# Performance work log

Measured on AMD Instinct MI355X. Metric: run time of the kernel, lower is better.

Reference implementation:

```python
import jax, jax.numpy as jnp
import numpy as np

N_NODES = 100000
N_EDGES = 3200000
D_IN = 256
D_HID = 256
D_OUT = 64


def setup_inputs() -> dict:
    key = jax.random.key(0)
    k1, k2, k3, k4 = jax.random.split(key, 4)
    x = jax.random.normal(k1, (N_NODES, D_IN), dtype=jnp.float32)
    edge_index = jax.random.randint(k2, (2, N_EDGES), 0, N_NODES, dtype=jnp.int32)
    W1 = jax.random.normal(k3, (D_IN, D_HID), dtype=jnp.float32) / np.sqrt(D_IN)
    b1 = jnp.zeros((D_HID,), dtype=jnp.float32)
    W2 = jax.random.normal(k4, (D_HID, D_OUT), dtype=jnp.float32) / np.sqrt(D_HID)
    b2 = jnp.zeros((D_OUT,), dtype=jnp.float32)
    return {"x": x, "edge_index": edge_index, "W1": W1, "b1": b1, "W2": W2, "b2": b2}


def _gcn_conv(x, src, dst, norm, W, b, n_nodes):
    # dense linear transform, then normalized scatter-add aggregation
    h = x @ W  # [N, out]
    msg = norm[:, None] * h[src]  # gather + scale, [E+N, out]
    out = jax.ops.segment_sum(msg, dst, num_segments=n_nodes)
    return out + b


def reference(x, edge_index, W1, b1, W2, b2):
    n = x.shape[0]
    # add self-loops (PyG GCNConv default)
    loops = jnp.arange(n, dtype=edge_index.dtype)
    src = jnp.concatenate([edge_index[0], loops])
    dst = jnp.concatenate([edge_index[1], loops])
    # symmetric normalization deg^{-1/2}[src] * deg^{-1/2}[dst]
    deg = jax.ops.segment_sum(jnp.ones_like(src, dtype=x.dtype), dst, num_segments=n)
    dinv = jnp.where(deg > 0, jax.lax.rsqrt(jnp.maximum(deg, 1.0)), 0.0)
    norm = dinv[src] * dinv[dst]

    h = _gcn_conv(x, src, dst, norm, W1, b1, n)
    h = jax.nn.relu(h)
    # dropout is identity at inference
    h = _gcn_conv(h, src, dst, norm, W2, b2, n)
    return jax.nn.log_softmax(h, axis=1)
```

## Files before the change

kernel.cpp:

```cpp
#include <hip/hip_runtime.h>
#include <hip/hip_bf16.h>


typedef __bf16 bf16;
typedef bf16 bf16x4 __attribute__((ext_vector_type(4)));
typedef bf16 bf16x8 __attribute__((ext_vector_type(8)));
typedef float f32x4 __attribute__((ext_vector_type(4)));
typedef signed char s8;

#define NBLK 256

__global__ __launch_bounds__(256) void k_b1(const int* __restrict__ edge, int E, int chunk,
                                            int NB, int* __restrict__ gcnt) {
    __shared__ int cnt[512];
    int tid = threadIdx.x;
    for (int i = tid; i < NB; i += 256) cnt[i] = 0;
    __syncthreads();
    int s = blockIdx.x * chunk, e = min(s + chunk, E);
    for (int i = s + tid; i < e; i += 256) atomicAdd(&cnt[edge[E + i] >> 9], 1);
    __syncthreads();
    for (int i = tid; i < NB; i += 256) gcnt[blockIdx.x * NB + i] = cnt[i];
}

__global__ void k_b2(const int* __restrict__ gcnt, int NB, int E, int* __restrict__ bstart) {
    __shared__ int col[256];
    int k = threadIdx.x;
    int sum = 0;
    if (k < NB)
        for (int b = 0; b < NBLK; ++b) sum += gcnt[b * NB + k];
    col[k] = sum;
    __syncthreads();
    for (int o = 1; o < 256; o <<= 1) {
        int v = (k >= o) ? col[k - o] : 0;
        __syncthreads();
        col[k] += v;
        __syncthreads();
    }
    if (k < NB) bstart[k] = col[k] - sum;
    if (k == 0) bstart[NB] = E;
}

__global__ void k_b2b(int* __restrict__ gcnt, int NB, const int* __restrict__ bstart) {
    __shared__ int col[256];
    int b = threadIdx.x;
    int k = blockIdx.x;
    int v = gcnt[b * NB + k];
    col[b] = v;
    __syncthreads();
    for (int o = 1; o < 256; o <<= 1) {
        int t = (b >= o) ? col[b - o] : 0;
        __syncthreads();
        col[b] += t;
        __syncthreads();
    }
    gcnt[b * NB + k] = bstart[k] + col[b] - v;
}

__global__ __launch_bounds__(256) void k_b3(const int* __restrict__ edge, int E, int chunk,
                                            int NB, const int* __restrict__ base,
                                            int* __restrict__ ebuf) {
    __shared__ int cnt[512];
    __shared__ int bs[512];
    int tid = threadIdx.x;
    for (int i = tid; i < NB; i += 256) {
        cnt[i] = 0;
        bs[i] = base[blockIdx.x * NB + i];
    }
    __syncthreads();
    int s = blockIdx.x * chunk, e = min(s + chunk, E);
    for (int i = s + tid; i < e; i += 256) {
        int sv = edge[i], dv = edge[E + i];
        int k = dv >> 9;
        int r = atomicAdd(&cnt[k], 1);
        ebuf[bs[k] + r] = sv | ((dv & 511) << 17);
    }
}

__global__ __launch_bounds__(256) void k_b45(const int* __restrict__ ebuf,
                                             const int* __restrict__ bstart,
                                             const float* __restrict__ scale, int n, int E,
                                             int NB, int* __restrict__ off,
                                             float* __restrict__ dinv,
                                             float* __restrict__ ws) {
    __shared__ int cnt[512];
    __shared__ int red[256];
    int tid = threadIdx.x;
    int k = blockIdx.x;
    cnt[tid] = 0;
    cnt[tid + 256] = 0;
    __syncthreads();
    int s = bstart[k], e = bstart[k + 1];
    for (int i = s + tid; i < e; i += 256) atomicAdd(&cnt[(ebuf[i] >> 17) & 511], 1);
    __syncthreads();
    int c0 = cnt[tid * 2], c1 = cnt[tid * 2 + 1];
    int sum = c0 + c1;
    red[tid] = sum;
    __syncthreads();
    for (int o = 1; o < 256; o <<= 1) {
        int v = (tid >= o) ? red[tid - o] : 0;
        __syncthreads();
        red[tid] += v;
        __syncthreads();
    }
    int ex = red[tid] - sum;
    int base = k << 9;
    int g0 = base + tid * 2, g1 = g0 + 1;
    int o0 = s + ex, o1 = s + ex + c0;
    if (g0 < n) {
        off[g0] = o0;
        float d0 = rsqrtf((float)(c0 + 1));
        dinv[g0] = d0;
        ws[g0] = d0 * scale[g0];
    } else if (g0 == n) off[g0] = o0;
    if (g1 < n) {
        off[g1] = o1;
        float d1 = rsqrtf((float)(c1 + 1));
        dinv[g1] = d1;
        ws[g1] = d1 * scale[g1];
    } else if (g1 == n) off[g1] = o1;
    if (k == NB - 1 && tid == 0) off[n] = E;
}

__global__ __launch_bounds__(256) void k_b6(const int* __restrict__ ebuf,
                                            const int* __restrict__ bstart,
                                            const int* __restrict__ off,
                                            const float* __restrict__ ws, int n,
                                            int2* __restrict__ pair) {
    __shared__ int cnt[512];
    __shared__ int offl[512];
    int tid = threadIdx.x;
    int k = blockIdx.x;
    int base = k << 9;
    cnt[tid] = 0;
    cnt[tid + 256] = 0;
    offl[tid] = (base + tid < n) ? off[base + tid] : 0;
    offl[tid + 256] = (base + 256 + tid < n) ? off[base + 256 + tid] : 0;
    __syncthreads();
    int s = bstart[k], e = bstart[k + 1];
    for (int i = s + tid; i < e; i += 256) {
        int pk = ebuf[i];
        int sv = pk & 0x1ffff;
        int node = (pk >> 17) & 511;
        int r = atomicAdd(&cnt[node], 1);
        pair[offl[node] + r] = make_int2(sv, __float_as_int(ws[sv]));
    }
}

__global__ __launch_bounds__(256) void k_quant(const float* __restrict__ x,
                                               unsigned char* __restrict__ xq,
                                               float* __restrict__ scale, int n) {
    int row = blockIdx.x * 4 + (threadIdx.x >> 6);
    int lane = threadIdx.x & 63;
    if (row >= n) return;
    f32x4 v = ((const f32x4*)x)[(size_t)row * 64 + lane];
    float m = fmaxf(fmaxf(fabsf(v[0]), fabsf(v[1])), fmaxf(fabsf(v[2]), fabsf(v[3])));
    for (int o = 32; o > 0; o >>= 1) m = fmaxf(m, __shfl_xor(m, o));
    m = fmaxf(m, 1e-20f);
    float inv = 127.0f / m;
    int b0 = (__float2int_rn(v[0] * inv) + 128) & 255;
    int b1 = (__float2int_rn(v[1] * inv) + 128) & 255;
    int b2 = (__float2int_rn(v[2] * inv) + 128) & 255;
    int b3 = (__float2int_rn(v[3] * inv) + 128) & 255;
    ((int*)xq)[(size_t)row * 64 + lane] = b0 | (b1 << 8) | (b2 << 16) | (b3 << 24);
    if (lane == 0) scale[row] = m / 127.0f;
}

__global__ __launch_bounds__(256) void k_quant2(const bf16* __restrict__ tb,
                                                const float* __restrict__ scale,
                                                unsigned char* __restrict__ tq,
                                                float* __restrict__ tscale,
                                                float* __restrict__ r2, int n) {
    int t = blockIdx.x * 256 + threadIdx.x;
    int row = t >> 3;
    int l8 = t & 7;
    if (row >= n) return;
    bf16x8 v = ((const bf16x8*)tb)[(size_t)row * 8 + l8];
    float f[8], m = 0.0f;
#pragma unroll
    for (int j = 0; j < 8; ++j) { f[j] = (float)v[j]; m = fmaxf(m, fabsf(f[j])); }
    for (int o = 4; o > 0; o >>= 1) m = fmaxf(m, __shfl_xor(m, o));
    m = fmaxf(m, 1e-20f);
    float inv = 127.0f / m;
    int lo = 0, hi = 0;
#pragma unroll
    for (int j = 0; j < 4; ++j) lo |= ((__float2int_rn(f[j] * inv) + 128) & 255) << (8 * j);
#pragma unroll
    for (int j = 0; j < 4; ++j) hi |= ((__float2int_rn(f[4 + j] * inv) + 128) & 255) << (8 * j);
    ((int2*)tq)[(size_t)row * 8 + l8] = make_int2(lo, hi);
    if (l8 == 0) {
        float s = m / 127.0f;
        tscale[row] = s;
        r2[row] = s / scale[row];
    }
}

__global__ void k_wt(const float* __restrict__ W, bf16* __restrict__ Wt, int NC) {
    int nc = blockIdx.x;
    int k = threadIdx.x;
    Wt[nc * 256 + k] = (bf16)W[k * NC + nc];
}

__device__ __forceinline__ void acc16(float a[16], uint4 t, float w, float& wsum) {
    wsum += w;
    unsigned u0 = t.x, u1 = t.y, u2 = t.z, u3 = t.w;
    a[0]  += w * (float)(u0 & 255u);
    a[1]  += w * (float)((u0 >> 8) & 255u);
    a[2]  += w * (float)((u0 >> 16) & 255u);
    a[3]  += w * (float)(u0 >> 24);
    a[4]  += w * (float)(u1 & 255u);
    a[5]  += w * (float)((u1 >> 8) & 255u);
    a[6]  += w * (float)((u1 >> 16) & 255u);
    a[7]  += w * (float)(u1 >> 24);
    a[8]  += w * (float)(u2 & 255u);
    a[9]  += w * (float)((u2 >> 8) & 255u);
    a[10] += w * (float)((u2 >> 16) & 255u);
    a[11] += w * (float)(u2 >> 24);
    a[12] += w * (float)(u3 & 255u);
    a[13] += w * (float)((u3 >> 8) & 255u);
    a[14] += w * (float)((u3 >> 16) & 255u);
    a[15] += w * (float)(u3 >> 24);
}

__device__ __forceinline__ void acc8(float a[8], int2 t, float w, float& wsum) {
    wsum += w;
    unsigned u0 = (unsigned)t.x, u1 = (unsigned)t.y;
    a[0] += w * (float)(u0 & 255u);
    a[1] += w * (float)((u0 >> 8) & 255u);
    a[2] += w * (float)((u0 >> 16) & 255u);
    a[3] += w * (float)(u0 >> 24);
    a[4] += w * (float)(u1 & 255u);
    a[5] += w * (float)((u1 >> 8) & 255u);
    a[6] += w * (float)((u1 >> 16) & 255u);
    a[7] += w * (float)(u1 >> 24);
}

__global__ __launch_bounds__(256) void k_agg1(const unsigned char* __restrict__ xq,
                                              const float* __restrict__ scale,
                                              const int* __restrict__ off,
                                              const int2* __restrict__ pair,
                                              const float* __restrict__ dinv,
                                              bf16* __restrict__ ax, int n) {
    int wv = blockIdx.x * 4 + (threadIdx.x >> 6);
    int lane = threadIdx.x & 63;
    int node = wv * 4 + (lane >> 4);
    int l16 = lane & 15;
    if (node >= n) return;
    int s0 = off[node], s1 = off[node + 1];
    float dv = dinv[node];
    float a[16] = {};
    float wsum = 0.0f;
    uint4 xs = *(const uint4*)(xq + (size_t)node * 256 + l16 * 16);
    acc16(a, xs, dv * scale[node], wsum);
    int e = s0;
    if (s1 - s0 >= 4) {
        int2 p[4];
#pragma unroll
        for (int q = 0; q < 4; ++q) p[q] = pair[s0 + q];
        e = s0 + 4;
        for (; e + 4 <= s1; e += 4) {
            uint4 t[4];
#pragma unroll
            for (int q = 0; q < 4; ++q)
                t[q] = *(const uint4*)(xq + (size_t)p[q].x * 256 + l16 * 16);
            int2 pn[4];
#pragma unroll
            for (int q = 0; q < 4; ++q) pn[q] = pair[e + q];
#pragma unroll
            for (int q = 0; q < 4; ++q) acc16(a, t[q], __int_as_float(p[q].y), wsum);
#pragma unroll
            for (int q = 0; q < 4; ++q) p[q] = pn[q];
        }
        uint4 t[4];
#pragma unroll
        for (int q = 0; q < 4; ++q)
            t[q] = *(const uint4*)(xq + (size_t)p[q].x * 256 + l16 * 16);
#pragma unroll
        for (int q = 0; q < 4; ++q) acc16(a, t[q], __int_as_float(p[q].y), wsum);
    }
    for (; e < s1; ++e) {
        int2 p = pair[e];
        uint4 t = *(const uint4*)(xq + (size_t)p.x * 256 + l16 * 16);
        acc16(a, t, __int_as_float(p.y), wsum);
    }
    float c = 128.0f * wsum;
    bf16x8 o0, o1;
#pragma unroll
    for (int j = 0; j < 8; ++j) o0[j] = (bf16)((a[j] - c) * dv);
#pragma unroll
    for (int j = 0; j < 8; ++j) o1[j] = (bf16)((a[8 + j] - c) * dv);
    ((bf16x8*)ax)[(size_t)node * 32 + l16 * 2] = o0;
    ((bf16x8*)ax)[(size_t)node * 32 + l16 * 2 + 1] = o1;
}

__device__ __forceinline__ int swz(int s) { return s ^ ((s >> 3) & 7); }

__global__ __launch_bounds__(256) void k_gemmp(const bf16* __restrict__ A,
                                               const bf16* __restrict__ Bt,
                                               const float* __restrict__ bias,
                                               bf16* __restrict__ C, int n) {
    __shared__ __align__(16) bf16 As[4 * 64 * 8];
    __shared__ __align__(16) bf16 Bs[16 * 64 * 8];
    int tid = threadIdx.x;
    int bm = blockIdx.x * 64;
    int w = tid >> 6, lane = tid & 63;

    int r = tid >> 2;
    int cq = tid & 3;
    int a_slot = swz(((r >> 4) * 64) + cq * 16 + (r & 15));
    int arow = bm + r; if (arow > n - 1) arow = n - 1;

    f32x4 acc[16] = {};

    for (int k0 = 0; k0 < 256; k0 += 32) {
        __syncthreads();
        uint4 av = *(const uint4*)(A + (size_t)arow * 256 + k0 + cq * 8);
        *(uint4*)(As + a_slot * 8) = av;
#pragma unroll
        for (int rep = 0; rep < 4; ++rep) {
            int r2 = rep * 64 + r;
            uint4 bv = *(const uint4*)(Bt + (size_t)r2 * 256 + k0 + cq * 8);
            *(uint4*)(Bs + swz(((r2 >> 4) * 64) + cq * 16 + (r2 & 15)) * 8) = bv;
        }
        __syncthreads();
        bf16x8 af = *(const bf16x8*)(As + swz(w * 64 + lane) * 8);
#pragma unroll
        for (int ct = 0; ct < 16; ++ct) {
            bf16x8 bfr = *(const bf16x8*)(Bs + swz(ct * 64 + lane) * 8);
            acc[ct] = __builtin_amdgcn_mfma_f32_16x16x32_bf16(af, bfr, acc[ct], 0, 0, 0);
        }
    }

    int colb = lane & 15, rowq = lane >> 4;
#pragma unroll
    for (int ct = 0; ct < 16; ++ct) {
        int col = ct * 16 + colb;
        float bv = bias[col];
#pragma unroll
        for (int rr = 0; rr < 4; ++rr) {
            int row = bm + w * 16 + rowq * 4 + rr;
            if (row < n) {
                float v = acc[ct][rr] + bv;
                C[(size_t)row * 256 + col] = (bf16)(v > 0.0f ? v : 0.0f);
            }
        }
    }
}

__global__ __launch_bounds__(256) void k_gemm2(const bf16* __restrict__ A,
                                               const bf16* __restrict__ Bt,
                                               bf16* __restrict__ C, int n) {
    __shared__ __align__(16) bf16 As[4 * 64 * 8];
    __shared__ __align__(16) bf16 Bs[4 * 64 * 8];
    int tid = threadIdx.x;
    int bm = blockIdx.x * 64;
    int w = tid >> 6, lane = tid & 63;
    int wm = w >> 1, wn = w & 1;

    int r = tid >> 2;
    int cq = tid & 3;
    int lds_slot = swz(((r >> 4) * 64) + cq * 16 + (r & 15));
    int arow = bm + r; if (arow > n - 1) arow = n - 1;

    f32x4 acc[2][2] = {};

    for (int k0 = 0; k0 < 256; k0 += 32) {
        __syncthreads();
        uint4 av = *(const uint4*)(A + (size_t)arow * 256 + k0 + cq * 8);
        uint4 bv = *(const uint4*)(Bt + (size_t)r * 256 + k0 + cq * 8);
        *(uint4*)(As + lds_slot * 8) = av;
        *(uint4*)(Bs + lds_slot * 8) = bv;
        __syncthreads();
#pragma unroll
        for (int i = 0; i < 2; ++i) {
            bf16x8 af = *(const bf16x8*)(As + swz((wm * 2 + i) * 64 + lane) * 8);
#pragma unroll
            for (int j = 0; j < 2; ++j) {
                bf16x8 bfr = *(const bf16x8*)(Bs + swz((wn * 2 + j) * 64 + lane) * 8);
                acc[i][j] = __builtin_amdgcn_mfma_f32_16x16x32_bf16(af, bfr, acc[i][j], 0, 0, 0);
            }
        }
    }

    int colb = lane & 15, rowq = lane >> 4;
#pragma unroll
    for (int i = 0; i < 2; ++i) {
#pragma unroll
        for (int j = 0; j < 2; ++j) {
            int col = wn * 32 + j * 16 + colb;
#pragma unroll
            for (int rr = 0; rr < 4; ++rr) {
                int row = bm + wm * 32 + i * 16 + rowq * 4 + rr;
                if (row < n) C[(size_t)row * 64 + col] = (bf16)acc[i][j][rr];
            }
        }
    }
}

__global__ __launch_bounds__(256) void k_agg2(const unsigned char* __restrict__ tq,
                                              const float* __restrict__ tscale,
                                              const float* __restrict__ r2,
                                              const int* __restrict__ off,
                                              const int2* __restrict__ pair,
                                              const float* __restrict__ dinv,
                                              const float* __restrict__ b2,
                                              float* __restrict__ out, int n) {
    int wv = blockIdx.x * 4 + (threadIdx.x >> 6);
    int lane = threadIdx.x & 63;
    int node = wv * 8 + (lane >> 3);
    int l8 = lane & 7;
    if (node >= n) return;
    int s0 = off[node], s1 = off[node + 1];
    float dv = dinv[node];
    const int2* T = (const int2*)tq;
    int2 ts = T[(size_t)node * 8 + l8];
    float a[8] = {};
    float wsum = 0.0f;
    acc8(a, ts, dv * tscale[node], wsum);
    int e = s0;
    if (s1 - s0 >= 4) {
        int2 p[4]; float sc[4];
#pragma unroll
        for (int q = 0; q < 4; ++q) p[q] = pair[s0 + q];
#pragma unroll
        for (int q = 0; q < 4; ++q) sc[q] = r2[p[q].x];
        e = s0 + 4;
        for (; e + 4 <= s1; e += 4) {
            int2 t[4];
#pragma unroll
            for (int q = 0; q < 4; ++q) t[q] = T[(size_t)p[q].x * 8 + l8];
            int2 pn[4];
#pragma unroll
            for (int q = 0; q < 4; ++q) pn[q] = pair[e + q];
            float scn[4];
#pragma unroll
            for (int q = 0; q < 4; ++q) scn[q] = r2[pn[q].x];
#pragma unroll
            for (int q = 0; q < 4; ++q) acc8(a, t[q], __int_as_float(p[q].y) * sc[q], wsum);
#pragma unroll
            for (int q = 0; q < 4; ++q) { p[q] = pn[q]; sc[q] = scn[q]; }
        }
        int2 t[4];
#pragma unroll
        for (int q = 0; q < 4; ++q) t[q] = T[(size_t)p[q].x * 8 + l8];
#pragma unroll
        for (int q = 0; q < 4; ++q) acc8(a, t[q], __int_as_float(p[q].y) * sc[q], wsum);
    }
    for (; e < s1; ++e) {
        int2 p = pair[e];
        float w = __int_as_float(p.y) * r2[p.x];
        int2 t = T[(size_t)p.x * 8 + l8];
        acc8(a, t, w, wsum);
    }
    float c = 128.0f * wsum;
    const float4* B2 = (const float4*)b2;
    float4 bv0 = B2[l8 * 2], bv1 = B2[l8 * 2 + 1];
    a[0] = (a[0] - c) * dv + bv0.x; a[1] = (a[1] - c) * dv + bv0.y;
    a[2] = (a[2] - c) * dv + bv0.z; a[3] = (a[3] - c) * dv + bv0.w;
    a[4] = (a[4] - c) * dv + bv1.x; a[5] = (a[5] - c) * dv + bv1.y;
    a[6] = (a[6] - c) * dv + bv1.z; a[7] = (a[7] - c) * dv + bv1.w;
    float m = a[0];
#pragma unroll
    for (int j = 1; j < 8; ++j) m = fmaxf(m, a[j]);
    for (int o = 4; o > 0; o >>= 1) m = fmaxf(m, __shfl_xor(m, o));
    float s = 0.0f;
#pragma unroll
    for (int j = 0; j < 8; ++j) s += __expf(a[j] - m);
    for (int o = 4; o > 0; o >>= 1) s += __shfl_xor(s, o);
    float ls = m + __logf(s);
    f32x4 o0, o1;
    o0[0] = a[0] - ls; o0[1] = a[1] - ls; o0[2] = a[2] - ls; o0[3] = a[3] - ls;
    o1[0] = a[4] - ls; o1[1] = a[5] - ls; o1[2] = a[6] - ls; o1[3] = a[7] - ls;
    f32x4* O = (f32x4*)out;
    O[(size_t)node * 16 + l8 * 2] = o0;
    O[(size_t)node * 16 + l8 * 2 + 1] = o1;
}

extern "C" void kernel_launch(void* const* d_in, const int* in_sizes, int n_in,
                              void* d_out, int out_size, void* d_ws, size_t ws_size,
                              hipStream_t stream) {
    const float* x   = (const float*)d_in[0];
    const int*  edge = (const int*)d_in[1];
    const float* W1  = (const float*)d_in[2];
    const float* b1  = (const float*)d_in[3];
    const float* W2  = (const float*)d_in[4];
    const float* b2  = (const float*)d_in[5];
    float* out = (float*)d_out;

    int n = in_sizes[0] / 256;
    int E = in_sizes[1] / 2;
    int NB = (n + 511) >> 9;
    int chunk = (E + NBLK - 1) / NBLK;

    char* ws = (char*)d_ws;
    auto alloc = [&](size_t bytes) -> char* {
        char* p = ws;
        ws += (bytes + 255) & ~(size_t)255;
        return p;
    };
    int*   gcnt   = (int*)alloc((size_t)NBLK * NB * 4);
    int*   bstart = (int*)alloc((size_t)(NB + 1) * 4);
    int*   ebuf   = (int*)alloc((size_t)E * 4);
    float* dinv   = (float*)alloc((size_t)n * 4);
    float* wsv    = (float*)alloc((size_t)n * 4);
    int*   off    = (int*)alloc((size_t)(n + 1) * 4);
    int2*  pair   = (int2*)alloc((size_t)E * 8);
    unsigned char* xq = (unsigned char*)alloc((size_t)n * 256);
    float* scale  = (float*)alloc((size_t)n * 4);
    bf16*  ax     = (bf16*)alloc((size_t)n * 256 * 2);
    bf16*  h1     = (bf16*)alloc((size_t)n * 256 * 2);
    bf16*  tb     = (bf16*)alloc((size_t)n * 64 * 2);
    unsigned char* tq = (unsigned char*)alloc((size_t)n * 64);
    float* tscale = (float*)alloc((size_t)n * 4);
    float* r2     = (float*)alloc((size_t)n * 4);
    bf16*  W1t    = (bf16*)alloc(256 * 256 * 2);
    bf16*  W2t    = (bf16*)alloc(64 * 256 * 2);

    k_quant<<<(n + 3) / 4, 256, 0, stream>>>(x, xq, scale, n);

    k_b1<<<NBLK, 256, 0, stream>>>(edge, E, chunk, NB, gcnt);
    k_b2<<<1, 256, 0, stream>>>(gcnt, NB, E, bstart);
    k_b2b<<<NB, 256, 0, stream>>>(gcnt, NB, bstart);
    k_b3<<<NBLK, 256, 0, stream>>>(edge, E, chunk, NB, gcnt, ebuf);
    k_b45<<<NB, 256, 0, stream>>>(ebuf, bstart, scale, n, E, NB, off, dinv, wsv);
    k_b6<<<NB, 256, 0, stream>>>(ebuf, bstart, off, wsv, n, pair);

    k_wt<<<256, 256, 0, stream>>>(W1, W1t, 256);
    k_wt<<<64, 256, 0, stream>>>(W2, W2t, 64);

    k_agg1<<<(n + 15) / 16, 256, 0, stream>>>(xq, scale, off, pair, dinv, ax, n);
    k_gemmp<<<(n + 63) / 64, 256, 0, stream>>>(ax, W1t, b1, h1, n);

    k_gemm2<<<(n + 63) / 64, 256, 0, stream>>>(h1, W2t, tb, n);
    k_quant2<<<(n * 8 + 255) / 256, 256, 0, stream>>>(tb, scale, tq, tscale, r2, n);
    k_agg2<<<(n + 31) / 32, 256, 0, stream>>>(tq, tscale, r2, off, pair, dinv, b2, out, n);
}
```

Before: 543.8 us.

## Add nontemporal loads/stores, pre-shift pair indices, packed f32x2 FMA, fold layer-2 weights

```diff
diff --git a/kernel.cpp b/kernel.cpp
--- a/kernel.cpp
+++ b/kernel.cpp
@@ -3,10 +3,10 @@
 
 
 typedef __bf16 bf16;
-typedef bf16 bf16x4 __attribute__((ext_vector_type(4)));
 typedef bf16 bf16x8 __attribute__((ext_vector_type(8)));
 typedef float f32x4 __attribute__((ext_vector_type(4)));
-typedef signed char s8;
+typedef float f32x2 __attribute__((ext_vector_type(2)));
+typedef int i32x2 __attribute__((ext_vector_type(2)));
 
 #define NBLK 256
 
@@ -72,7 +72,7 @@
         int sv = edge[i], dv = edge[E + i];
         int k = dv >> 9;
         int r = atomicAdd(&cnt[k], 1);
-        ebuf[bs[k] + r] = sv | ((dv & 511) << 17);
+        __builtin_nontemporal_store(sv | ((dv & 511) << 17), &ebuf[bs[k] + r]);
     }
 }
 
@@ -90,7 +90,10 @@
     cnt[tid + 256] = 0;
     __syncthreads();
     int s = bstart[k], e = bstart[k + 1];
-    for (int i = s + tid; i < e; i += 256) atomicAdd(&cnt[(ebuf[i] >> 17) & 511], 1);
+    for (int i = s + tid; i < e; i += 256) {
+        int pk = __builtin_nontemporal_load(&ebuf[i]);
+        atomicAdd(&cnt[(pk >> 17) & 511], 1);
+    }
     __syncthreads();
     int c0 = cnt[tid * 2], c1 = cnt[tid * 2 + 1];
     int sum = c0 + c1;
@@ -125,7 +128,7 @@
                                             const int* __restrict__ bstart,
                                             const int* __restrict__ off,
                                             const float* __restrict__ ws, int n,
-                                            int2* __restrict__ pair) {
+                                            i32x2* __restrict__ pair) {
     __shared__ int cnt[512];
     __shared__ int offl[512];
     int tid = threadIdx.x;
@@ -138,11 +141,14 @@
     __syncthreads();
     int s = bstart[k], e = bstart[k + 1];
     for (int i = s + tid; i < e; i += 256) {
-        int pk = ebuf[i];
+        int pk = __builtin_nontemporal_load(&ebuf[i]);
         int sv = pk & 0x1ffff;
         int node = (pk >> 17) & 511;
         int r = atomicAdd(&cnt[node], 1);
-        pair[offl[node] + r] = make_int2(sv, __float_as_int(ws[sv]));
+        i32x2 pv;
+        pv[0] = sv << 8;
+        pv[1] = __float_as_int(ws[sv]);
+        __builtin_nontemporal_store(pv, &pair[offl[node] + r]);
     }
 }
 
@@ -152,7 +158,7 @@
     int row = blockIdx.x * 4 + (threadIdx.x >> 6);
     int lane = threadIdx.x & 63;
     if (row >= n) return;
-    f32x4 v = ((const f32x4*)x)[(size_t)row * 64 + lane];
+    f32x4 v = __builtin_nontemporal_load(((const f32x4*)x) + (size_t)row * 64 + lane);
     float m = fmaxf(fmaxf(fabsf(v[0]), fabsf(v[1])), fmaxf(fabsf(v[2]), fabsf(v[3])));
     for (int o = 32; o > 0; o >>= 1) m = fmaxf(m, __shfl_xor(m, o));
     m = fmaxf(m, 1e-20f);
@@ -166,10 +172,9 @@
 }
 
 __global__ __launch_bounds__(256) void k_quant2(const bf16* __restrict__ tb,
-                                                const float* __restrict__ scale,
+                                                const float* __restrict__ dinv,
                                                 unsigned char* __restrict__ tq,
-                                                float* __restrict__ tscale,
-                                                float* __restrict__ r2, int n) {
+                                                float* __restrict__ w2v, int n) {
     int t = blockIdx.x * 256 + threadIdx.x;
     int row = t >> 3;
     int l8 = t & 7;
@@ -186,12 +191,9 @@
     for (int j = 0; j < 4; ++j) lo |= ((__float2int_rn(f[j] * inv) + 128) & 255) << (8 * j);
 #pragma unroll
     for (int j = 0; j < 4; ++j) hi |= ((__float2int_rn(f[4 + j] * inv) + 128) & 255) << (8 * j);
-    ((int2*)tq)[(size_t)row * 8 + l8] = make_int2(lo, hi);
-    if (l8 == 0) {
-        float s = m / 127.0f;
-        tscale[row] = s;
-        r2[row] = s / scale[row];
-    }
+    i32x2 qv; qv[0] = lo; qv[1] = hi;
+    ((i32x2*)tq)[(size_t)row * 8 + l8] = qv;
+    if (l8 == 0) w2v[row] = dinv[row] * (m / 127.0f);
 }
 
 __global__ void k_wt(const float* __restrict__ W, bf16* __restrict__ Wt, int NC) {
@@ -200,44 +202,36 @@
     Wt[nc * 256 + k] = (bf16)W[k * NC + nc];
 }
 
-__device__ __forceinline__ void acc16(float a[16], uint4 t, float w, float& wsum) {
+__device__ __forceinline__ void acc16(f32x2 a[8], uint4 t, float w, float& wsum) {
     wsum += w;
+    f32x2 w2 = {w, w};
     unsigned u0 = t.x, u1 = t.y, u2 = t.z, u3 = t.w;
-    a[0]  += w * (float)(u0 & 255u);
-    a[1]  += w * (float)((u0 >> 8) & 255u);
-    a[2]  += w * (float)((u0 >> 16) & 255u);
-    a[3]  += w * (float)(u0 >> 24);
-    a[4]  += w * (float)(u1 & 255u);
-    a[5]  += w * (float)((u1 >> 8) & 255u);
-    a[6]  += w * (float)((u1 >> 16) & 255u);
-    a[7]  += w * (float)(u1 >> 24);
-    a[8]  += w * (float)(u2 & 255u);
-    a[9]  += w * (float)((u2 >> 8) & 255u);
-    a[10] += w * (float)((u2 >> 16) & 255u);
-    a[11] += w * (float)(u2 >> 24);
-    a[12] += w * (float)(u3 & 255u);
-    a[13] += w * (float)((u3 >> 8) & 255u);
-    a[14] += w * (float)((u3 >> 16) & 255u);
-    a[15] += w * (float)(u3 >> 24);
-}
-
-__device__ __forceinline__ void acc8(float a[8], int2 t, float w, float& wsum) {
+    f32x2 c;
+    c[0] = (float)(u0 & 255u);         c[1] = (float)((u0 >> 8) & 255u);  a[0] += w2 * c;
+    c[0] = (float)((u0 >> 16) & 255u); c[1] = (float)(u0 >> 24);         a[1] += w2 * c;
+    c[0] = (float)(u1 & 255u);         c[1] = (float)((u1 >> 8) & 255u);  a[2] += w2 * c;
+    c[0] = (float)((u1 >> 16) & 255u); c[1] = (float)(u1 >> 24);         a[3] += w2 * c;
+    c[0] = (float)(u2 & 255u);         c[1] = (float)((u2 >> 8) & 255u);  a[4] += w2 * c;
+    c[0] = (float)((u2 >> 16) & 255u); c[1] = (float)(u2 >> 24);         a[5] += w2 * c;
+    c[0] = (float)(u3 & 255u);         c[1] = (float)((u3 >> 8) & 255u);  a[6] += w2 * c;
+    c[0] = (float)((u3 >> 16) & 255u); c[1] = (float)(u3 >> 24);         a[7] += w2 * c;
+}
+
+__device__ __forceinline__ void acc8(f32x2 a[4], i32x2 t, float w, float& wsum) {
     wsum += w;
-    unsigned u0 = (unsigned)t.x, u1 = (unsigned)t.y;
-    a[0] += w * (float)(u0 & 255u);
-    a[1] += w * (float)((u0 >> 8) & 255u);
-    a[2] += w * (float)((u0 >> 16) & 255u);
-    a[3] += w * (float)(u0 >> 24);
-    a[4] += w * (float)(u1 & 255u);
-    a[5] += w * (float)((u1 >> 8) & 255u);
-    a[6] += w * (float)((u1 >> 16) & 255u);
-    a[7] += w * (float)(u1 >> 24);
+    f32x2 w2 = {w, w};
+    unsigned u0 = (unsigned)t[0], u1 = (unsigned)t[1];
+    f32x2 c;
+    c[0] = (float)(u0 & 255u);         c[1] = (float)((u0 >> 8) & 255u);  a[0] += w2 * c;
+    c[0] = (float)((u0 >> 16) & 255u); c[1] = (float)(u0 >> 24);         a[1] += w2 * c;
+    c[0] = (float)(u1 & 255u);         c[1] = (float)((u1 >> 8) & 255u);  a[2] += w2 * c;
+    c[0] = (float)((u1 >> 16) & 255u); c[1] = (float)(u1 >> 24);         a[3] += w2 * c;
 }
 
 __global__ __launch_bounds__(256) void k_agg1(const unsigned char* __restrict__ xq,
-                                              const float* __restrict__ scale,
+                                              const float* __restrict__ wsv,
                                               const int* __restrict__ off,
-                                              const int2* __restrict__ pair,
+                                              const i32x2* __restrict__ pair,
                                               const float* __restrict__ dinv,
                                               bf16* __restrict__ ax, int n) {
     int wv = blockIdx.x * 4 + (threadIdx.x >> 6);
@@ -247,49 +241,53 @@
     if (node >= n) return;
     int s0 = off[node], s1 = off[node + 1];
     float dv = dinv[node];
-    float a[16] = {};
+    const unsigned char* xqb = xq + l16 * 16;
+    f32x2 a[8] = {};
     float wsum = 0.0f;
-    uint4 xs = *(const uint4*)(xq + (size_t)node * 256 + l16 * 16);
-    acc16(a, xs, dv * scale[node], wsum);
+    uint4 xs = *(const uint4*)(xqb + (size_t)node * 256);
+    acc16(a, xs, wsv[node], wsum);
     int e = s0;
     if (s1 - s0 >= 4) {
-        int2 p[4];
-#pragma unroll
-        for (int q = 0; q < 4; ++q) p[q] = pair[s0 + q];
+        i32x2 p[4];
+#pragma unroll
+        for (int q = 0; q < 4; ++q) p[q] = __builtin_nontemporal_load(&pair[s0 + q]);
         e = s0 + 4;
         for (; e + 4 <= s1; e += 4) {
             uint4 t[4];
 #pragma unroll
             for (int q = 0; q < 4; ++q)
-                t[q] = *(const uint4*)(xq + (size_t)p[q].x * 256 + l16 * 16);
-            int2 pn[4];
-#pragma unroll
-            for (int q = 0; q < 4; ++q) pn[q] = pair[e + q];
-#pragma unroll
-            for (int q = 0; q < 4; ++q) acc16(a, t[q], __int_as_float(p[q].y), wsum);
+                t[q] = *(const uint4*)(xqb + (unsigned)p[q][0]);
+            i32x2 pn[4];
+#pragma unroll
+            for (int q = 0; q < 4; ++q) pn[q] = __builtin_nontemporal_load(&pair[e + q]);
+#pragma unroll
+            for (int q = 0; q < 4; ++q) acc16(a, t[q], __int_as_float(p[q][1]), wsum);
 #pragma unroll
             for (int q = 0; q < 4; ++q) p[q] = pn[q];
         }
         uint4 t[4];
 #pragma unroll
         for (int q = 0; q < 4; ++q)
-            t[q] = *(const uint4*)(xq + (size_t)p[q].x * 256 + l16 * 16);
-#pragma unroll
-        for (int q = 0; q < 4; ++q) acc16(a, t[q], __int_as_float(p[q].y), wsum);
+            t[q] = *(const uint4*)(xqb + (unsigned)p[q][0]);
+#pragma unroll
+        for (int q = 0; q < 4; ++q) acc16(a, t[q], __int_as_float(p[q][1]), wsum);
     }
     for (; e < s1; ++e) {
-        int2 p = pair[e];
-        uint4 t = *(const uint4*)(xq + (size_t)p.x * 256 + l16 * 16);
-        acc16(a, t, __int_as_float(p.y), wsum);
+        i32x2 p = __builtin_nontemporal_load(&pair[e]);
+        uint4 t = *(const uint4*)(xqb + (unsigned)p[0]);
+        acc16(a, t, __int_as_float(p[1]), wsum);
     }
     float c = 128.0f * wsum;
     bf16x8 o0, o1;
 #pragma unroll
-    for (int j = 0; j < 8; ++j) o0[j] = (bf16)((a[j] - c) * dv);
-#pragma unroll
-    for (int j = 0; j < 8; ++j) o1[j] = (bf16)((a[8 + j] - c) * dv);
-    ((bf16x8*)ax)[(size_t)node * 32 + l16 * 2] = o0;
-    ((bf16x8*)ax)[(size_t)node * 32 + l16 * 2 + 1] = o1;
+    for (int j = 0; j < 4; ++j) {
+        o0[2 * j]     = (bf16)((a[j][0] - c) * dv);
+        o0[2 * j + 1] = (bf16)((a[j][1] - c) * dv);
+        o1[2 * j]     = (bf16)((a[4 + j][0] - c) * dv);
+        o1[2 * j + 1] = (bf16)((a[4 + j][1] - c) * dv);
+    }
+    __builtin_nontemporal_store(o0, ((bf16x8*)ax) + (size_t)node * 32 + l16 * 2);
+    __builtin_nontemporal_store(o1, ((bf16x8*)ax) + (size_t)node * 32 + l16 * 2 + 1);
 }
 
 __device__ __forceinline__ int swz(int s) { return s ^ ((s >> 3) & 7); }
@@ -397,10 +395,9 @@
 }
 
 __global__ __launch_bounds__(256) void k_agg2(const unsigned char* __restrict__ tq,
-                                              const float* __restrict__ tscale,
-                                              const float* __restrict__ r2,
+                                              const float* __restrict__ w2v,
                                               const int* __restrict__ off,
-                                              const int2* __restrict__ pair,
+                                              const i32x2* __restrict__ pair,
                                               const float* __restrict__ dinv,
                                               const float* __restrict__ b2,
                                               float* __restrict__ out, int n) {
@@ -411,68 +408,71 @@
     if (node >= n) return;
     int s0 = off[node], s1 = off[node + 1];
     float dv = dinv[node];
-    const int2* T = (const int2*)tq;
-    int2 ts = T[(size_t)node * 8 + l8];
-    float a[8] = {};
+    const unsigned char* tqb = tq + l8 * 8;
+    i32x2 ts = *(const i32x2*)(tqb + (size_t)node * 64);
+    f32x2 a[4] = {};
     float wsum = 0.0f;
-    acc8(a, ts, dv * tscale[node], wsum);
+    acc8(a, ts, w2v[node], wsum);
     int e = s0;
     if (s1 - s0 >= 4) {
-        int2 p[4]; float sc[4];
-#pragma unroll
-        for (int q = 0; q < 4; ++q) p[q] = pair[s0 + q];
-#pragma unroll
-        for (int q = 0; q < 4; ++q) sc[q] = r2[p[q].x];
+        i32x2 p[4]; float sc[4];
+#pragma unroll
+        for (int q = 0; q < 4; ++q) p[q] = __builtin_nontemporal_load(&pair[s0 + q]);
+#pragma unroll
+        for (int q = 0; q < 4; ++q) sc[q] = w2v[(unsigned)p[q][0] >> 8];
         e = s0 + 4;
         for (; e + 4 <= s1; e += 4) {
-            int2 t[4];
-#pragma unroll
-            for (int q = 0; q < 4; ++q) t[q] = T[(size_t)p[q].x * 8 + l8];
-            int2 pn[4];
-#pragma unroll
-            for (int q = 0; q < 4; ++q) pn[q] = pair[e + q];
+            i32x2 t[4];
+#pragma unroll
+            for (int q = 0; q < 4; ++q) t[q] = *(const i32x2*)(tqb + ((unsigned)p[q][0] >> 2));
+            i32x2 pn[4];
+#pragma unroll
+            for (int q = 0; q < 4; ++q) pn[q] = __builtin_nontemporal_load(&pair[e + q]);
             float scn[4];
 #pragma unroll
-            for (int q = 0; q < 4; ++q) scn[q] = r2[pn[q].x];
-#pragma unroll
-            for (int q = 0; q < 4; ++q) acc8(a, t[q], __int_as_float(p[q].y) * sc[q], wsum);
+            for (int q = 0; q < 4; ++q) scn[q] = w2v[(unsigned)pn[q][0] >> 8];
+#pragma unroll
+            for (int q = 0; q < 4; ++q) acc8(a, t[q], sc[q], wsum);
 #pragma unroll
             for (int q = 0; q < 4; ++q) { p[q] = pn[q]; sc[q] = scn[q]; }
         }
-        int2 t[4];
-#pragma unroll
-        for (int q = 0; q < 4; ++q) t[q] = T[(size_t)p[q].x * 8 + l8];
-#pragma unroll
-        for (int q = 0; q < 4; ++q) acc8(a, t[q], __int_as_float(p[q].y) * sc[q], wsum);
+        i32x2 t[4];
+#pragma unroll
+        for (int q = 0; q < 4; ++q) t[q] = *(const i32x2*)(tqb + ((unsigned)p[q][0] >> 2));
+#pragma unroll
+        for (int q = 0; q < 4; ++q) acc8(a, t[q], sc[q], wsum);
     }
     for (; e < s1; ++e) {
-        int2 p = pair[e];
-        float w = __int_as_float(p.y) * r2[p.x];
-        int2 t = T[(size_t)p.x * 8 + l8];
+        i32x2 p = __builtin_nontemporal_load(&pair[e]);
+        float w = w2v[(unsigned)p[0] >> 8];
+        i32x2 t = *(const i32x2*)(tqb + ((unsigned)p[0] >> 2));
         acc8(a, t, w, wsum);
     }
     float c = 128.0f * wsum;
+    float aa[8];
+#pragma unroll
+    for (int j = 0; j < 4; ++j) { aa[2 * j] = a[j][0]; aa[2 * j + 1] = a[j][1]; }
     const float4* B2 = (const float4*)b2;
     float4 bv0 = B2[l8 * 2], bv1 = B2[l8 * 2 + 1];
-    a[0] = (a[0] - c) * dv + bv0.x; a[1] = (a[1] - c) * dv + bv0.y;
-    a[2] = (a[2] - c) * dv + bv0.z; a[3] = (a[3] - c) * dv + bv0.w;
-    a[4] = (a[4] - c) * dv + bv1.x; a[5] = (a[5] - c) * dv + bv1.y;
-    a[6] = (a[6] - c) * dv + bv1.z; a[7] = (a[7] - c) * dv + bv1.w;
-    float m = a[0];
-#pragma unroll
-    for (int j = 1; j < 8; ++j) m = fmaxf(m, a[j]);
+    aa[0] = (aa[0] - c) * dv + bv0.x; aa[1] = (aa[1] - c) * dv + bv0.y;
+    aa[2] = (aa[2] - c) * dv + bv0.z; aa[3] = (aa[3] - c) * dv + bv0.w;
+    aa[4] = (aa[4] - c) * dv + bv1.x; aa[5] = (aa[5] - c) * dv + bv1.y;
+    aa[6] = (aa[6] - c) * dv + bv1.z; aa[7] = (aa[7] - c) * dv + bv1.w;
+    float m = aa[0];
+#pragma unroll
+    for (int j = 1; j < 8; ++j) m = fmaxf(m, aa[j]);
     for (int o = 4; o > 0; o >>= 1) m = fmaxf(m, __shfl_xor(m, o));
     float s = 0.0f;
 #pragma unroll
-    for (int j = 0; j < 8; ++j) s += __expf(a[j] - m);
+    for (int j = 0; j < 8; ++j) s += __expf(aa[j] - m);
     for (int o = 4; o > 0; o >>= 1) s += __shfl_xor(s, o);
     float ls = m + __logf(s);
     f32x4 o0, o1;
-    o0[0] = a[0] - ls; o0[1] = a[1] - ls; o0[2] = a[2] - ls; o0[3] = a[3] - ls;
-    o1[0] = a[4] - ls; o1[1] = a[5] - ls; o1[2] = a[6] - ls; o1[3] = a[7] - ls;
+    o0[0] = aa[0] - ls; o0[1] = aa[1] - ls; o0[2] = aa[2] - ls; o0[3] = aa[3] - ls;
+    o1[0] = aa[4] - ls; o1[1] = aa[5] - ls; o1[2] = aa[6] - ls; o1[3] = aa[7] - ls;
     f32x4* O = (f32x4*)out;
-    O[(size_t)node * 16 + l8 * 2] = o0;
-    O[(size_t)node * 16 + l8 * 2 + 1] = o1;
+    __builtin_nontemporal_store(o0, O + (size_t)node * 16 + l8 * 2);
+    __builtin_nontemporal_store(o1, O + (size_t)node * 16 + l8 * 2 + 1);
 }
 
 extern "C" void kernel_launch(void* const* d_in, const int* in_sizes, int n_in,
@@ -503,15 +503,14 @@
     float* dinv   = (float*)alloc((size_t)n * 4);
     float* wsv    = (float*)alloc((size_t)n * 4);
     int*   off    = (int*)alloc((size_t)(n + 1) * 4);
-    int2*  pair   = (int2*)alloc((size_t)E * 8);
+    i32x2* pair   = (i32x2*)alloc((size_t)E * 8);
     unsigned char* xq = (unsigned char*)alloc((size_t)n * 256);
     float* scale  = (float*)alloc((size_t)n * 4);
     bf16*  ax     = (bf16*)alloc((size_t)n * 256 * 2);
     bf16*  h1     = (bf16*)alloc((size_t)n * 256 * 2);
     bf16*  tb     = (bf16*)alloc((size_t)n * 64 * 2);
     unsigned char* tq = (unsigned char*)alloc((size_t)n * 64);
-    float* tscale = (float*)alloc((size_t)n * 4);
-    float* r2     = (float*)alloc((size_t)n * 4);
+    float* w2v    = (float*)alloc((size_t)n * 4);
     bf16*  W1t    = (bf16*)alloc(256 * 256 * 2);
     bf16*  W2t    = (bf16*)alloc(64 * 256 * 2);
 
@@ -527,10 +526,10 @@
     k_wt<<<256, 256, 0, stream>>>(W1, W1t, 256);
     k_wt<<<64, 256, 0, stream>>>(W2, W2t, 64);
 
-    k_agg1<<<(n + 15) / 16, 256, 0, stream>>>(xq, scale, off, pair, dinv, ax, n);
+    k_agg1<<<(n + 15) / 16, 256, 0, stream>>>(xq, wsv, off, pair, dinv, ax, n);
     k_gemmp<<<(n + 63) / 64, 256, 0, stream>>>(ax, W1t, b1, h1, n);
 
     k_gemm2<<<(n + 63) / 64, 256, 0, stream>>>(h1, W2t, tb, n);
-    k_quant2<<<(n * 8 + 255) / 256, 256, 0, stream>>>(tb, scale, tq, tscale, r2, n);
-    k_agg2<<<(n + 31) / 32, 256, 0, stream>>>(tq, tscale, r2, off, pair, dinv, b2, out, n);
-}
+    k_quant2<<<(n * 8 + 255) / 256, 256, 0, stream>>>(tb, dinv, tq, w2v, n);
+    k_agg2<<<(n + 31) / 32, 256, 0, stream>>>(tq, w2v, off, pair, dinv, b2, out, n);
+}
```

Result: slower. 725.3 us (+33.4%).
